# Performance work log

Measured on AMD Instinct MI355X. Metric: run time of the kernel, lower is better.

Reference implementation:

```python
import jax, jax.numpy as jnp
import numpy as np

BATCH, SEQ_LEN, HIDDEN, NUM_SENTS = 16, 4096, 1024, 32


def setup_inputs() -> dict:
    key = jax.random.key(0)
    k1, k2 = jax.random.split(key)
    last_hidden_state = jax.random.normal(k1, (BATCH, SEQ_LEN, HIDDEN), dtype=jnp.float32)
    sentence_mask = jax.random.randint(k2, (BATCH, SEQ_LEN), 0, NUM_SENTS, dtype=jnp.int64)
    return {
        "last_hidden_state": last_hidden_state,
        "sentence_mask": sentence_mask,
        "num_sents": NUM_SENTS,
    }


def reference(last_hidden_state, sentence_mask, num_sents):
    # unique sentence ids; assume ids 0..num_sents-1 all occur (static shape)
    unique_sents = jnp.arange(num_sents, dtype=sentence_mask.dtype)
    # one-hot segment membership: (batch, num_sents, seq_len)
    masks = (sentence_mask[:, None, :] == unique_sents[None, :, None])
    counts = masks.sum(axis=2).astype(last_hidden_state.dtype)  # (batch, num_sents)
    # segment-sum via contraction over seq_len -> (batch, num_sents, hidden);
    # avoids the torch (B, S, L, H) broadcasted intermediate
    sums = jnp.einsum("bsl,blh->bsh", masks.astype(last_hidden_state.dtype), last_hidden_state)
    sentence_embeddings = sums / counts[:, :, None]
    return sentence_embeddings, unique_sents
```

## Files before the change

kernel.cpp:

```cpp
#include <hip/hip_runtime.h>


#define BATCH   16
#define SEQ     4096
#define HIDDEN  1024
#define NSENT   32
#define CHUNK   256
#define NCHUNK  (HIDDEN / CHUNK)
#define KSPLIT  8
#define SEG     (SEQ / KSPLIT)
#define EMB_ELEMS (BATCH * NSENT * HIDDEN)

__global__ __launch_bounds__(256) void count_kernel(const int* __restrict__ mask,
                                                    float* __restrict__ counts) {
    __shared__ int c[NSENT];
    const int b   = blockIdx.x;
    const int tid = threadIdx.x;
    if (tid < NSENT) c[tid] = 0;
    __syncthreads();
    for (int i = tid; i < SEQ; i += 256) {
        atomicAdd(&c[mask[b * SEQ + i] & (NSENT - 1)], 1);
    }
    __syncthreads();
    if (tid < NSENT) counts[b * NSENT + tid] = (float)c[tid];
}

__global__ __launch_bounds__(256) void accum_kernel(const float* __restrict__ x,
                                                    const int* __restrict__ mask,
                                                    float* __restrict__ sums) {
    __shared__ float acc[NSENT][CHUNK];
    __shared__ int   smask[SEG];

    const int tid   = threadIdx.x;
    const int blk   = blockIdx.x;
    const int b     = blk / (NCHUNK * KSPLIT);
    const int rem   = blk % (NCHUNK * KSPLIT);
    const int chunk = rem / KSPLIT;
    const int split = rem % KSPLIT;

    #pragma unroll
    for (int s = 0; s < NSENT; ++s) acc[s][tid] = 0.0f;

    const int l0 = split * SEG;
    for (int i = tid; i < SEG; i += 256)
        smask[i] = mask[b * SEQ + l0 + i] & (NSENT - 1);
    __syncthreads();

    const float* xp = x + (size_t)(b * SEQ + l0) * HIDDEN + chunk * CHUNK + tid;
    #pragma unroll 8
    for (int i = 0; i < SEG; ++i) {
        acc[smask[i]][tid] += xp[(size_t)i * HIDDEN];
    }
    __syncthreads();

    float* dst = sums + (size_t)b * NSENT * HIDDEN + chunk * CHUNK + tid;
    #pragma unroll
    for (int s = 0; s < NSENT; ++s) {
        atomicAdd(dst + s * HIDDEN, acc[s][tid]);
    }
}

__global__ __launch_bounds__(256) void finalize_kernel(float* __restrict__ out,
                                                       const float* __restrict__ counts) {
    const int idx = blockIdx.x * 256 + threadIdx.x;
    const float c = counts[idx >> 10];
    out[idx] = out[idx] / c;
    if (idx < NSENT) out[EMB_ELEMS + idx] = (float)idx;
}

extern "C" void kernel_launch(void* const* d_in, const int* in_sizes, int n_in,
                              void* d_out, int out_size, void* d_ws, size_t ws_size,
                              hipStream_t stream) {
    const float* x    = (const float*)d_in[0];
    const int*   mask = (const int*)d_in[1];
    float*       out  = (float*)d_out;
    float*       counts = (float*)d_ws;

    hipMemsetAsync(out, 0, (size_t)EMB_ELEMS * sizeof(float), stream);

    count_kernel<<<BATCH, 256, 0, stream>>>(mask, counts);
    accum_kernel<<<BATCH * NCHUNK * KSPLIT, 256, 0, stream>>>(x, mask, out);
    finalize_kernel<<<EMB_ELEMS / 256, 256, 0, stream>>>(out, counts);
}
```

Baseline: 372.5 us.

## Replace scatter-accumulate with counting-sort permutation and per-sentence gather reduction

A prep kernel counting-sorts the sequence positions of each batch by sentence id, producing a permutation and per-sentence offsets. A gather kernel then has each block read only the rows of its sentence with float4 loads, accumulate in registers, and write the mean directly. This removes the memset, the LDS read-modify-write accumulators, the global atomics and the separate finalize pass. In exchange the x rows are read in scattered order, only 1024 blocks of 128 threads run, and a sentence with zero tokens would produce a division by zero as before.

```diff
diff --git a/kernel.cpp b/kernel.cpp
--- a/kernel.cpp
+++ b/kernel.cpp
@@ -5,67 +5,90 @@
 #define SEQ     4096
 #define HIDDEN  1024
 #define NSENT   32
-#define CHUNK   256
-#define NCHUNK  (HIDDEN / CHUNK)
-#define KSPLIT  8
-#define SEG     (SEQ / KSPLIT)
 #define EMB_ELEMS (BATCH * NSENT * HIDDEN)
 
-__global__ __launch_bounds__(256) void count_kernel(const int* __restrict__ mask,
-                                                    float* __restrict__ counts) {
-    __shared__ int c[NSENT];
+#define CHUNK2   512
+#define NCHUNK2  (HIDDEN / CHUNK2)
+#define GTHREADS 128
+
+__global__ __launch_bounds__(256) void prep_kernel(const int* __restrict__ mask,
+                                                   int* __restrict__ perm,
+                                                   int* __restrict__ offs,
+                                                   float* __restrict__ out) {
+    __shared__ int sm[SEQ];
+    __shared__ int cnt[NSENT];
+    __shared__ int pref[NSENT];
+    __shared__ int cursor[NSENT];
+
     const int b   = blockIdx.x;
     const int tid = threadIdx.x;
-    if (tid < NSENT) c[tid] = 0;
+
+    if (tid < NSENT) cnt[tid] = 0;
     __syncthreads();
+
+    #pragma unroll
     for (int i = tid; i < SEQ; i += 256) {
-        atomicAdd(&c[mask[b * SEQ + i] & (NSENT - 1)], 1);
+        const int s = mask[b * SEQ + i] & (NSENT - 1);
+        sm[i] = s;
+        atomicAdd(&cnt[s], 1);
     }
     __syncthreads();
-    if (tid < NSENT) counts[b * NSENT + tid] = (float)c[tid];
+
+    if (tid == 0) {
+        int run = 0;
+        #pragma unroll
+        for (int s = 0; s < NSENT; ++s) { pref[s] = run; run += cnt[s]; }
+    }
+    __syncthreads();
+
+    if (tid < NSENT) {
+        cursor[tid] = pref[tid];
+        offs[b * (NSENT + 1) + tid] = pref[tid];
+    }
+    if (tid == 0) offs[b * (NSENT + 1) + NSENT] = SEQ;
+    if (b == 0 && tid < NSENT) out[EMB_ELEMS + tid] = (float)tid;
+    __syncthreads();
+
+    for (int i = tid; i < SEQ; i += 256) {
+        const int s   = sm[i];
+        const int pos = atomicAdd(&cursor[s], 1);
+        perm[b * SEQ + pos] = i;
+    }
 }
 
-__global__ __launch_bounds__(256) void accum_kernel(const float* __restrict__ x,
-                                                    const int* __restrict__ mask,
-                                                    float* __restrict__ sums) {
-    __shared__ float acc[NSENT][CHUNK];
-    __shared__ int   smask[SEG];
+__global__ __launch_bounds__(GTHREADS) void gather_kernel(const float* __restrict__ x,
+                                                          const int* __restrict__ perm,
+                                                          const int* __restrict__ offs,
+                                                          float* __restrict__ out) {
+    __shared__ int sidx[SEQ];
 
     const int tid   = threadIdx.x;
     const int blk   = blockIdx.x;
-    const int b     = blk / (NCHUNK * KSPLIT);
-    const int rem   = blk % (NCHUNK * KSPLIT);
-    const int chunk = rem / KSPLIT;
-    const int split = rem % KSPLIT;
+    const int chunk = blk & (NCHUNK2 - 1);
+    const int s     = (blk >> 1) & (NSENT - 1);
+    const int b     = blk >> 6;
 
-    #pragma unroll
-    for (int s = 0; s < NSENT; ++s) acc[s][tid] = 0.0f;
+    const int base  = b * (NSENT + 1) + s;
+    const int start = offs[base];
+    const int n     = offs[base + 1] - start;
 
-    const int l0 = split * SEG;
-    for (int i = tid; i < SEG; i += 256)
-        smask[i] = mask[b * SEQ + l0 + i] & (NSENT - 1);
+    for (int j = tid; j < n; j += GTHREADS)
+        sidx[j] = perm[b * SEQ + start + j];
     __syncthreads();
 
-    const float* xp = x + (size_t)(b * SEQ + l0) * HIDDEN + chunk * CHUNK + tid;
+    const int c0 = chunk * CHUNK2 + tid * 4;
+    const float* xb = x + (size_t)b * SEQ * HIDDEN + c0;
+
+    float ax = 0.f, ay = 0.f, az = 0.f, aw = 0.f;
     #pragma unroll 8
-    for (int i = 0; i < SEG; ++i) {
-        acc[smask[i]][tid] += xp[(size_t)i * HIDDEN];
+    for (int k = 0; k < n; ++k) {
+        const float4 v = *(const float4*)(xb + (size_t)sidx[k] * HIDDEN);
+        ax += v.x; ay += v.y; az += v.z; aw += v.w;
     }
-    __syncthreads();
 
-    float* dst = sums + (size_t)b * NSENT * HIDDEN + chunk * CHUNK + tid;
-    #pragma unroll
-    for (int s = 0; s < NSENT; ++s) {
-        atomicAdd(dst + s * HIDDEN, acc[s][tid]);
-    }
-}
-
-__global__ __launch_bounds__(256) void finalize_kernel(float* __restrict__ out,
-                                                       const float* __restrict__ counts) {
-    const int idx = blockIdx.x * 256 + threadIdx.x;
-    const float c = counts[idx >> 10];
-    out[idx] = out[idx] / c;
-    if (idx < NSENT) out[EMB_ELEMS + idx] = (float)idx;
+    const float inv = 1.0f / (float)n;
+    float4 r; r.x = ax * inv; r.y = ay * inv; r.z = az * inv; r.w = aw * inv;
+    *(float4*)(out + (size_t)(b * NSENT + s) * HIDDEN + c0) = r;
 }
 
 extern "C" void kernel_launch(void* const* d_in, const int* in_sizes, int n_in,
@@ -74,11 +97,10 @@
     const float* x    = (const float*)d_in[0];
     const int*   mask = (const int*)d_in[1];
     float*       out  = (float*)d_out;
-    float*       counts = (float*)d_ws;
 
-    hipMemsetAsync(out, 0, (size_t)EMB_ELEMS * sizeof(float), stream);
+    int* perm = (int*)d_ws;
+    int* offs = perm + BATCH * SEQ;
 
-    count_kernel<<<BATCH, 256, 0, stream>>>(mask, counts);
-    accum_kernel<<<BATCH * NCHUNK * KSPLIT, 256, 0, stream>>>(x, mask, out);
-    finalize_kernel<<<EMB_ELEMS / 256, 256, 0, stream>>>(out, counts);
+    prep_kernel<<<BATCH, 256, 0, stream>>>(mask, perm, offs, out);
+    gather_kernel<<<BATCH * NSENT * NCHUNK2, GTHREADS, 0, stream>>>(x, perm, offs, out);
 }
```

Result: no change. 371.9 us (-0.2%).
